# Kernel tuning notes

Hardware: AMD Instinct MI355X
Metric: run time of the kernel (lower is better)

Reference implementation:

```python
import jax, jax.numpy as jnp
import numpy as np

N_NODES = 100000
N_EDGES = 6400000


def setup_inputs() -> dict:
    key = jax.random.key(0)
    k = jax.random.split(key, 5)
    x = jax.random.normal(k[0], (N_NODES, 4), dtype=jnp.float32)
    edge_index = jax.random.randint(k[1], (2, N_EDGES), 0, N_NODES, dtype=jnp.int32)
    # Glorot-style init for GCN linear weights
    W1 = jax.random.normal(k[2], (4, 16), dtype=jnp.float32) * (1.0 / np.sqrt(4.0))
    b1 = jnp.zeros((16,), dtype=jnp.float32)
    W2 = jax.random.normal(k[3], (16, 2), dtype=jnp.float32) * (1.0 / np.sqrt(16.0))
    b2 = jnp.zeros((2,), dtype=jnp.float32)
    return {"x": x, "edge_index": edge_index, "W1": W1, "b1": b1, "W2": W2, "b2": b2}


def _gcn_conv(x, src, dst, deg_inv_sqrt, W, b):
    """One GCNConv layer: linear transform -> symmetric-normalized scatter-add -> bias.

    src, dst already include self-loops; deg_inv_sqrt precomputed on the
    self-loop-augmented graph (matches PyG GCNConv defaults).
    """
    n = x.shape[0]
    h = x @ W                                   # [N, F_out]
    coef = deg_inv_sqrt[src] * deg_inv_sqrt[dst]  # [E+N]
    msg = h[src] * coef[:, None]                # gather + scale, [E+N, F_out]
    out = jax.ops.segment_sum(msg, dst, num_segments=n)  # scatter-add
    return out + b


def reference(x, edge_index, W1, b1, W2, b2):
    n = x.shape[0]
    loop = jnp.arange(n, dtype=edge_index.dtype)
    src = jnp.concatenate([edge_index[0], loop])  # add self-loops
    dst = jnp.concatenate([edge_index[1], loop])
    deg = jax.ops.segment_sum(jnp.ones_like(dst, dtype=x.dtype), dst, num_segments=n)
    deg_inv_sqrt = jnp.where(deg > 0, jax.lax.rsqrt(deg), 0.0)

    h = jax.nn.relu(_gcn_conv(x, src, dst, deg_inv_sqrt, W1, b1))
    return _gcn_conv(h, src, dst, deg_inv_sqrt, W2, b2)
```

## Files before the change

### kernel.cpp

```cpp
#include <hip/hip_runtime.h>

#define TPB 256
#define CSH 10
#define CN 1024
#define NBC_MAX 128
#define STILE 8192
#define EPT (STILE / TPB)

#define B20 1048576
#define S1F 131072.0f
#define S2F 8192.0f

typedef unsigned long long u64;

__device__ __forceinline__ unsigned enc_fx(float v, float scale) {
    int xi = __float2int_rn(v * scale);
    xi = max(-(B20 - 1), min(B20 - 1, xi));
    return (unsigned)(xi + B20);
}

__global__ void k_zero(int* __restrict__ p, int n) {
    int i = blockIdx.x * blockDim.x + threadIdx.x;
    if (i < n) p[i] = 0;
}

__global__ void k_passCk(const int* __restrict__ src, const int* __restrict__ dst,
                         unsigned* __restrict__ packed, int* __restrict__ chunkl,
                         int* __restrict__ chunkp, int E, int NBC) {
    __shared__ unsigned stage[STILE];
    __shared__ int cnt[NBC_MAX], lb[NBC_MAX];
    int tb = blockIdx.x * STILE;
    int te = min(E, tb + STILE);
    if (threadIdx.x < NBC_MAX) cnt[threadIdx.x] = 0;
    __syncthreads();
    unsigned pk[EPT];
    int br[EPT];
#pragma unroll
    for (int u = 0; u < EPT; u++) {
        int i = tb + u * TPB + (int)threadIdx.x;
        br[u] = -1;
        if (i < te) {
            int d = dst[i];
            int b = d >> CSH;
            pk[u] = ((unsigned)src[i] << CSH) | (unsigned)(d & (CN - 1));
            int r = atomicAdd(&cnt[b], 1);
            br[u] = b | (r << 7);
        }
    }
    __syncthreads();
    if (threadIdx.x < (unsigned)NBC) {
        int b = threadIdx.x;
        int sum = 0;
        for (int j = 0; j < b; j++) sum += cnt[j];
        lb[b] = sum;
        chunkl[blockIdx.x * NBC + b] = cnt[b];
        chunkp[blockIdx.x * NBC + b] = tb + sum;
    }
    __syncthreads();
#pragma unroll
    for (int u = 0; u < EPT; u++) {
        if (br[u] >= 0) {
            int b = br[u] & (NBC_MAX - 1);
            stage[lb[b] + (br[u] >> 7)] = pk[u];
        }
    }
    __syncthreads();
    for (int i = threadIdx.x; i < te - tb; i += TPB)
        packed[tb + i] = stage[i];
}

__global__ void k_degk(const unsigned* __restrict__ packed, const int* __restrict__ chunkl,
                       const int* __restrict__ chunkp, int* __restrict__ deg,
                       int SD, int ntiles, int NBC, int N) {
    __shared__ int cnt[CN];
    for (int i = threadIdx.x; i < CN; i += TPB) cnt[i] = 0;
    __syncthreads();
    int b = blockIdx.x / SD, s = blockIdx.x - b * SD;
    int wv = threadIdx.x >> 6, lane = threadIdx.x & 63;
    for (int t = s * 4 + wv; t < ntiles; t += SD * 4) {
        int len = chunkl[t * NBC + b];
        if (!len) continue;
        int pos = chunkp[t * NBC + b];
        for (int i = lane; i < len; i += 64)
            atomicAdd(&cnt[packed[pos + i] & (CN - 1)], 1);
    }
    __syncthreads();
    int node0 = b << CSH;
    for (int i = threadIdx.x; i < CN; i += TPB)
        if (cnt[i] && node0 + i < N) atomicAdd(&deg[node0 + i], cnt[i]);
}

__global__ void k_prepv(const float* __restrict__ x, const int* __restrict__ deg,
                        float* __restrict__ xs, unsigned* __restrict__ xse, int N) {
    int v = blockIdx.x * blockDim.x + threadIdx.x;
    if (v >= N) return;
    float di = rsqrtf((float)(deg[v] + 1));
    float4 xv = ((const float4*)x)[v];
    xv.x *= di; xv.y *= di; xv.z *= di; xv.w *= di;
    ((float4*)xs)[v] = xv;
    uint4 e;
    e.x = enc_fx(xv.x, S1F); e.y = enc_fx(xv.y, S1F);
    e.z = enc_fx(xv.z, S1F); e.w = enc_fx(xv.w, S1F);
    ((uint4*)xse)[v] = e;
}

__global__ void k_agg1k(const unsigned* __restrict__ packed, const int* __restrict__ chunkl,
                        const int* __restrict__ chunkp, const unsigned* __restrict__ xse,
                        u64* __restrict__ partial1, int S1, int ntiles, int NBC) {
    __shared__ u64 acc[CN * 3];
    for (int i = threadIdx.x; i < CN * 3; i += TPB) acc[i] = 0ULL;
    __syncthreads();
    int b = blockIdx.x / S1, s = blockIdx.x - b * S1;
    int wv = threadIdx.x >> 6, lane = threadIdx.x & 63;
    for (int t = s * 4 + wv; t < ntiles; t += S1 * 4) {
        int len = chunkl[t * NBC + b];
        if (!len) continue;
        int pos = chunkp[t * NBC + b];
        for (int i = lane; i < len; i += 64) {
            unsigned pk = packed[pos + i];
            uint4 g = ((const uint4*)xse)[pk >> CSH];
            int n = pk & (CN - 1);
            atomicAdd(&acc[n * 3 + 0], (u64)g.x | ((u64)g.y << 32));
            atomicAdd(&acc[n * 3 + 1], (u64)g.z | ((u64)g.w << 32));
        }
    }
    __syncthreads();
    u64* p = partial1 + (size_t)blockIdx.x * (CN * 2);
    for (int i = threadIdx.x; i < CN * 2; i += TPB)
        p[i] = acc[(i >> 1) * 3 + (i & 1)];
}

__global__ void k_comb1q(const u64* __restrict__ partial1,
                         const float* __restrict__ xs, const int* __restrict__ deg,
                         const float* __restrict__ W1, const float* __restrict__ b1,
                         const float* __restrict__ W2,
                         float* __restrict__ hs2f, unsigned* __restrict__ hs2e,
                         int S1, int N) {
    __shared__ float w1[64], w2[32], bb[16];
    if (threadIdx.x < 64) w1[threadIdx.x] = W1[threadIdx.x];
    if (threadIdx.x < 32) w2[threadIdx.x] = W2[threadIdx.x];
    if (threadIdx.x < 16) bb[threadIdx.x] = b1[threadIdx.x];
    __syncthreads();
    int v = blockIdx.x * blockDim.x + threadIdx.x;
    if (v >= N) return;
    int b = v >> CSH, lv = v & (CN - 1);
    u64 a01 = 0, a23 = 0;
    for (int s = 0; s < S1; s++) {
        const u64* q = partial1 + ((size_t)(b * S1 + s) * CN + lv) * 2;
        a01 += q[0];
        a23 += q[1];
    }
    int dg = deg[v];
    long long bias = (long long)dg << 20;
    const float inv = 1.0f / S1F;
    float f0 = (float)((long long)(a01 & 0xffffffffULL) - bias) * inv;
    float f1 = (float)((long long)(a01 >> 32) - bias) * inv;
    float f2 = (float)((long long)(a23 & 0xffffffffULL) - bias) * inv;
    float f3 = (float)((long long)(a23 >> 32) - bias) * inv;
    float4 self = ((const float4*)xs)[v];
    float di = rsqrtf((float)(dg + 1));
    float v0 = (f0 + self.x) * di, v1 = (f1 + self.y) * di;
    float v2 = (f2 + self.z) * di, v3 = (f3 + self.w) * di;
    float s0 = 0.f, s1 = 0.f;
#pragma unroll
    for (int j = 0; j < 16; j++) {
        float h = v0 * w1[j] + v1 * w1[16 + j] + v2 * w1[32 + j] + v3 * w1[48 + j] + bb[j];
        h = fmaxf(h, 0.0f);
        s0 += h * w2[2 * j];
        s1 += h * w2[2 * j + 1];
    }
    s0 *= di; s1 *= di;
    ((float2*)hs2f)[v] = make_float2(s0, s1);
    uint2 e;
    e.x = enc_fx(s0, S2F);
    e.y = enc_fx(s1, S2F);
    ((uint2*)hs2e)[v] = e;
}

__global__ void k_agg2k(const unsigned* __restrict__ packed, const int* __restrict__ chunkl,
                        const int* __restrict__ chunkp, const unsigned* __restrict__ hs2e,
                        u64* __restrict__ partial2, int S2, int ntiles, int NBC) {
    __shared__ u64 acc[CN];
    for (int i = threadIdx.x; i < CN; i += TPB) acc[i] = 0ULL;
    __syncthreads();
    int b = blockIdx.x / S2, s = blockIdx.x - b * S2;
    int wv = threadIdx.x >> 6, lane = threadIdx.x & 63;
    for (int t = s * 4 + wv; t < ntiles; t += S2 * 4) {
        int len = chunkl[t * NBC + b];
        if (!len) continue;
        int pos = chunkp[t * NBC + b];
        for (int i = lane; i < len; i += 64) {
            unsigned pk = packed[pos + i];
            uint2 g = ((const uint2*)hs2e)[pk >> CSH];
            atomicAdd(&acc[pk & (CN - 1)], (u64)g.x | ((u64)g.y << 32));
        }
    }
    __syncthreads();
    u64* p = partial2 + (size_t)blockIdx.x * CN;
    for (int i = threadIdx.x; i < CN; i += TPB) p[i] = acc[i];
}

__global__ void k_comb2q(const u64* __restrict__ partial2,
                         const float* __restrict__ hs2f, const int* __restrict__ deg,
                         const float* __restrict__ b2, float* __restrict__ out,
                         int S2, int N) {
    int v = blockIdx.x * blockDim.x + threadIdx.x;
    if (v >= N) return;
    int b = v >> CSH, lv = v & (CN - 1);
    u64 t = 0;
    for (int s = 0; s < S2; s++)
        t += partial2[(size_t)(b * S2 + s) * CN + lv];
    int dg = deg[v];
    long long bias = (long long)dg << 20;
    const float inv = 1.0f / S2F;
    float f0 = (float)((long long)(t & 0xffffffffULL) - bias) * inv;
    float f1 = (float)((long long)(t >> 32) - bias) * inv;
    float2 self = ((const float2*)hs2f)[v];
    float di = rsqrtf((float)(dg + 1));
    ((float2*)out)[v] = make_float2((f0 + self.x) * di + b2[0],
                                    (f1 + self.y) * di + b2[1]);
}


__global__ void k_deg_fb(const int* __restrict__ dst, int* __restrict__ deg, int E) {
    int i = blockIdx.x * blockDim.x + threadIdx.x;
    if (i < E) atomicAdd(&deg[dst[i]], 1);
}
__global__ void k_dis_fb(const int* __restrict__ deg, float* __restrict__ dis, int N) {
    int v = blockIdx.x * blockDim.x + threadIdx.x;
    if (v < N) dis[v] = rsqrtf((float)(deg[v] + 1));
}
__global__ void k_lin1_fb(const float* __restrict__ x, const float* __restrict__ W1,
// ... 53 lines not shown
    int s = src[e], d = dst[e];
    float2 m = ((const float2*)hs2)[s];
    atomicAdd(&agg2[d * 2 + 0], m.x);
    atomicAdd(&agg2[d * 2 + 1], m.y);
}
__global__ void k_out_fb(const float* __restrict__ agg2, const float* __restrict__ dis,
                         const float* __restrict__ b2, float* __restrict__ out, int N) {
    int v = blockIdx.x * blockDim.x + threadIdx.x;
    if (v >= N) return;
    float d = dis[v];
    out[v * 2 + 0] = agg2[v * 2 + 0] * d + b2[0];
    out[v * 2 + 1] = agg2[v * 2 + 1] * d + b2[1];
}


extern "C" void kernel_launch(void* const* d_in, const int* in_sizes, int n_in,
                              void* d_out, int out_size, void* d_ws, size_t ws_size,
                              hipStream_t stream) {
    const float* x  = (const float*)d_in[0];
    const int*   ei = (const int*)d_in[1];
    const float* W1 = (const float*)d_in[2];
    const float* b1 = (const float*)d_in[3];
    const float* W2 = (const float*)d_in[4];
    const float* b2 = (const float*)d_in[5];

    const int N = in_sizes[0] / 4;
    const int E = in_sizes[1] / 2;
    const int* src = ei;
    const int* dst = ei + E;
    float* outp = (float*)d_out;

    auto align = [](size_t v) { return (v + 255) & ~(size_t)255; };
    const int NBC = (N + CN - 1) >> CSH;
    const int gN  = (N + TPB - 1) / TPB;
    const int ntiles = (E + STILE - 1) / STILE;
    const int SD = 8;
    const bool src_fits = (size_t)N <= ((size_t)1 << (32 - CSH));
    const bool fx_safe = (long long)E <= (long long)N * 512;

    const int S1 = 8, S2 = 16;
    size_t part_bytes  = (size_t)NBC * S1 * CN * 16;
    size_t part2_bytes = (size_t)NBC * S2 * CN * 8;
    size_t part_max = part_bytes > part2_bytes ? part_bytes : part2_bytes;

    size_t need_new = align((size_t)E * 4)
                    + align((size_t)N * 16)
                    + align((size_t)N * 16)
                    + align((size_t)N * 8)
                    + align((size_t)N * 8)
                    + align((size_t)N * 4)
                    + align((size_t)ntiles * NBC * 4)
                    + align((size_t)ntiles * NBC * 4)
                    + align(part_max);

    if (ws_size >= need_new && NBC <= NBC_MAX && src_fits && fx_safe) {
        char* ws = (char*)d_ws;
        unsigned* packed = (unsigned*)ws; ws += align((size_t)E * 4);
        float* xs    = (float*)ws;    ws += align((size_t)N * 16);
        unsigned* xse = (unsigned*)ws; ws += align((size_t)N * 16);
        float* hs2f  = (float*)ws;    ws += align((size_t)N * 8);
        unsigned* hs2e = (unsigned*)ws; ws += align((size_t)N * 8);
        int* deg     = (int*)ws;      ws += align((size_t)N * 4);
        int* chunkl  = (int*)ws;      ws += align((size_t)ntiles * NBC * 4);
        int* chunkp  = (int*)ws;      ws += align((size_t)ntiles * NBC * 4);
        u64* partial1 = (u64*)ws;
        u64* partial2 = (u64*)ws;

        k_zero<<<gN, TPB, 0, stream>>>(deg, N);
        k_passCk<<<ntiles, TPB, 0, stream>>>(src, dst, packed, chunkl, chunkp, E, NBC);
        k_degk<<<NBC * SD, TPB, 0, stream>>>(packed, chunkl, chunkp, deg, SD, ntiles, NBC, N);
        k_prepv<<<gN, TPB, 0, stream>>>(x, deg, xs, xse, N);
        k_agg1k<<<NBC * S1, TPB, 0, stream>>>(packed, chunkl, chunkp, xse, partial1, S1, ntiles, NBC);
        k_comb1q<<<gN, TPB, 0, stream>>>(partial1, xs, deg, W1, b1, W2, hs2f, hs2e, S1, N);
        k_agg2k<<<NBC * S2, TPB, 0, stream>>>(packed, chunkl, chunkp, hs2e, partial2, S2, ntiles, NBC);
        k_comb2q<<<gN, TPB, 0, stream>>>(partial2, hs2f, deg, b2, outp, S2, N);
    } else {
        char* ws = (char*)d_ws;
        int*   deg  = (int*)ws;   ws += align((size_t)N * 4);
        float* dis  = (float*)ws; ws += align((size_t)N * 4);
        float* hs1  = (float*)ws; ws += align((size_t)N * 16 * 4);
        float* agg1 = (float*)ws; ws += align((size_t)N * 16 * 4);
        float* hs2  = (float*)ws; ws += align((size_t)N * 2 * 4);
        float* agg2 = (float*)ws; ws += align((size_t)N * 2 * 4);
        int gE = (E + TPB - 1) / TPB;
        int gE4 = ((size_t)E * 4 + TPB - 1) / TPB;

        k_zero<<<gN, TPB, 0, stream>>>(deg, N);
        k_deg_fb<<<gE, TPB, 0, stream>>>(dst, deg, E);
        k_dis_fb<<<gN, TPB, 0, stream>>>(deg, dis, N);
        k_lin1_fb<<<gN, TPB, 0, stream>>>(x, W1, dis, hs1, agg1, N);
        k_scat1_fb<<<gE4, TPB, 0, stream>>>(src, dst, hs1, agg1, E * 4);
        k_lin2_fb<<<gN, TPB, 0, stream>>>(agg1, dis, b1, W2, hs2, agg2, N);
        k_scat2_fb<<<gE, TPB, 0, stream>>>(src, dst, hs2, agg2, E);
        k_out_fb<<<gN, TPB, 0, stream>>>(agg2, dis, b2, outp, N);
    }
}
```

Before: 241.1 us.

## Transpose chunk metadata, batch-load chunk descriptors, and unroll gathers for latency hiding

The chunk length and position tables are stored bucket-major so each wave reads a contiguous range of chunk descriptors. Waves load 64 descriptors at once, broadcast them with shuffles, and process two chunks per iteration with four independent packed and feature loads issued before the atomics. This is meant to hide gather latency by raising memory-level parallelism. It also doubles the split factors S1 and S2 when workspace allows, giving more blocks but larger partial buffers and more combine work.

```diff
diff --git a/kernel.cpp b/kernel.cpp
--- a/kernel.cpp
+++ b/kernel.cpp
@@ -25,8 +25,8 @@
 }
 
 __global__ void k_passCk(const int* __restrict__ src, const int* __restrict__ dst,
-                         unsigned* __restrict__ packed, int* __restrict__ chunkl,
-                         int* __restrict__ chunkp, int E, int NBC) {
+                         unsigned* __restrict__ packed, int* __restrict__ chunklT,
+                         int* __restrict__ chunkpT, int E, int NBC, int ntiles) {
     __shared__ unsigned stage[STILE];
     __shared__ int cnt[NBC_MAX], lb[NBC_MAX];
     int tb = blockIdx.x * STILE;
@@ -53,8 +53,8 @@
         int sum = 0;
         for (int j = 0; j < b; j++) sum += cnt[j];
         lb[b] = sum;
-        chunkl[blockIdx.x * NBC + b] = cnt[b];
-        chunkp[blockIdx.x * NBC + b] = tb + sum;
+        chunklT[(size_t)b * ntiles + blockIdx.x] = cnt[b];
+        chunkpT[(size_t)b * ntiles + blockIdx.x] = tb + sum;
     }
     __syncthreads();
 #pragma unroll
@@ -69,20 +69,45 @@
         packed[tb + i] = stage[i];
 }
 
-__global__ void k_degk(const unsigned* __restrict__ packed, const int* __restrict__ chunkl,
-                       const int* __restrict__ chunkp, int* __restrict__ deg,
-                       int SD, int ntiles, int NBC, int N) {
+
+__global__ void k_degk(const unsigned* __restrict__ packed, const int* __restrict__ chunklT,
+                       const int* __restrict__ chunkpT, int* __restrict__ deg,
+                       int SD, int ntiles, int E, int N) {
     __shared__ int cnt[CN];
     for (int i = threadIdx.x; i < CN; i += TPB) cnt[i] = 0;
     __syncthreads();
     int b = blockIdx.x / SD, s = blockIdx.x - b * SD;
     int wv = threadIdx.x >> 6, lane = threadIdx.x & 63;
-    for (int t = s * 4 + wv; t < ntiles; t += SD * 4) {
-        int len = chunkl[t * NBC + b];
-        if (!len) continue;
-        int pos = chunkp[t * NBC + b];
-        for (int i = lane; i < len; i += 64)
-            atomicAdd(&cnt[packed[pos + i] & (CN - 1)], 1);
+    int W = SD * 4, widx = s * 4 + wv;
+    int base = ntiles / W, rem = ntiles - base * W;
+    int q0 = widx * base + min(widx, rem);
+    int nch = base + (widx < rem ? 1 : 0);
+    const int* cl = chunklT + (size_t)b * ntiles;
+    const int* cp = chunkpT + (size_t)b * ntiles;
+    for (int jb = 0; jb < nch; jb += 64) {
+        int mylen = 0, mypos = 0;
+        if (jb + lane < nch) {
+            mylen = cl[q0 + jb + lane];
+            mypos = cp[q0 + jb + lane];
+        }
+        int jcnt = min(64, nch - jb);
+        for (int j = 0; j < jcnt; j += 2) {
+            int len0 = __shfl(mylen, j), pos0 = __shfl(mypos, j);
+            int len1 = 0, pos1 = 0;
+            if (j + 1 < jcnt) { len1 = __shfl(mylen, j + 1); pos1 = __shfl(mypos, j + 1); }
+            unsigned pk0a = packed[min(pos0 + lane,      E - 1)];
+            unsigned pk0b = packed[min(pos0 + 64 + lane, E - 1)];
+            unsigned pk1a = packed[min(pos1 + lane,      E - 1)];
+            unsigned pk1b = packed[min(pos1 + 64 + lane, E - 1)];
+            if (lane < len0)      atomicAdd(&cnt[pk0a & (CN - 1)], 1);
+            if (64 + lane < len0) atomicAdd(&cnt[pk0b & (CN - 1)], 1);
+            if (lane < len1)      atomicAdd(&cnt[pk1a & (CN - 1)], 1);
+            if (64 + lane < len1) atomicAdd(&cnt[pk1b & (CN - 1)], 1);
+            for (int i = 128 + lane; i < len0; i += 64)
+                atomicAdd(&cnt[packed[pos0 + i] & (CN - 1)], 1);
+            for (int i = 128 + lane; i < len1; i += 64)
+                atomicAdd(&cnt[packed[pos1 + i] & (CN - 1)], 1);
+        }
     }
     __syncthreads();
     int node0 = b << CSH;
@@ -104,24 +129,58 @@
     ((uint4*)xse)[v] = e;
 }
 
-__global__ void k_agg1k(const unsigned* __restrict__ packed, const int* __restrict__ chunkl,
-                        const int* __restrict__ chunkp, const unsigned* __restrict__ xse,
-                        u64* __restrict__ partial1, int S1, int ntiles, int NBC) {
+#define AGG1_AT(pkv, gv) { int n_ = (int)((pkv) & (CN - 1)) * 3; \
+    atomicAdd(&acc[n_],     (u64)(gv).x | ((u64)(gv).y << 32)); \
+    atomicAdd(&acc[n_ + 1], (u64)(gv).z | ((u64)(gv).w << 32)); }
+
+__global__ void k_agg1k(const unsigned* __restrict__ packed, const int* __restrict__ chunklT,
+                        const int* __restrict__ chunkpT, const unsigned* __restrict__ xse,
+                        u64* __restrict__ partial1, int S1, int ntiles, int E) {
     __shared__ u64 acc[CN * 3];
     for (int i = threadIdx.x; i < CN * 3; i += TPB) acc[i] = 0ULL;
     __syncthreads();
     int b = blockIdx.x / S1, s = blockIdx.x - b * S1;
     int wv = threadIdx.x >> 6, lane = threadIdx.x & 63;
-    for (int t = s * 4 + wv; t < ntiles; t += S1 * 4) {
-        int len = chunkl[t * NBC + b];
-        if (!len) continue;
-        int pos = chunkp[t * NBC + b];
-        for (int i = lane; i < len; i += 64) {
-            unsigned pk = packed[pos + i];
-            uint4 g = ((const uint4*)xse)[pk >> CSH];
-            int n = pk & (CN - 1);
-            atomicAdd(&acc[n * 3 + 0], (u64)g.x | ((u64)g.y << 32));
-            atomicAdd(&acc[n * 3 + 1], (u64)g.z | ((u64)g.w << 32));
+    int W = S1 * 4, widx = s * 4 + wv;
+    int base = ntiles / W, rem = ntiles - base * W;
+    int q0 = widx * base + min(widx, rem);
+    int nch = base + (widx < rem ? 1 : 0);
+    const int* cl = chunklT + (size_t)b * ntiles;
+    const int* cp = chunkpT + (size_t)b * ntiles;
+    const uint4* xse4 = (const uint4*)xse;
+    for (int jb = 0; jb < nch; jb += 64) {
+        int mylen = 0, mypos = 0;
+        if (jb + lane < nch) {
+            mylen = cl[q0 + jb + lane];
+            mypos = cp[q0 + jb + lane];
+        }
+        int jcnt = min(64, nch - jb);
+        for (int j = 0; j < jcnt; j += 2) {
+            int len0 = __shfl(mylen, j), pos0 = __shfl(mypos, j);
+            int len1 = 0, pos1 = 0;
+            if (j + 1 < jcnt) { len1 = __shfl(mylen, j + 1); pos1 = __shfl(mypos, j + 1); }
+            unsigned pk0a = packed[min(pos0 + lane,      E - 1)];
+            unsigned pk0b = packed[min(pos0 + 64 + lane, E - 1)];
+            unsigned pk1a = packed[min(pos1 + lane,      E - 1)];
+            unsigned pk1b = packed[min(pos1 + 64 + lane, E - 1)];
+            uint4 g0a = xse4[pk0a >> CSH];
+            uint4 g0b = xse4[pk0b >> CSH];
+            uint4 g1a = xse4[pk1a >> CSH];
+            uint4 g1b = xse4[pk1b >> CSH];
+            if (lane < len0)      AGG1_AT(pk0a, g0a);
+            if (64 + lane < len0) AGG1_AT(pk0b, g0b);
+            if (lane < len1)      AGG1_AT(pk1a, g1a);
+            if (64 + lane < len1) AGG1_AT(pk1b, g1b);
+            for (int i = 128 + lane; i < len0; i += 64) {
+                unsigned pk = packed[pos0 + i];
+                uint4 g = xse4[pk >> CSH];
+                AGG1_AT(pk, g);
+            }
+            for (int i = 128 + lane; i < len1; i += 64) {
+                unsigned pk = packed[pos1 + i];
+                uint4 g = xse4[pk >> CSH];
+                AGG1_AT(pk, g);
+            }
         }
     }
     __syncthreads();
@@ -177,22 +236,58 @@
     ((uint2*)hs2e)[v] = e;
 }
 
-__global__ void k_agg2k(const unsigned* __restrict__ packed, const int* __restrict__ chunkl,
-                        const int* __restrict__ chunkp, const unsigned* __restrict__ hs2e,
-                        u64* __restrict__ partial2, int S2, int ntiles, int NBC) {
+__global__ void k_agg2k(const unsigned* __restrict__ packed, const int* __restrict__ chunklT,
+                        const int* __restrict__ chunkpT, const unsigned* __restrict__ hs2e,
+                        u64* __restrict__ partial2, int S2, int ntiles, int E) {
     __shared__ u64 acc[CN];
     for (int i = threadIdx.x; i < CN; i += TPB) acc[i] = 0ULL;
     __syncthreads();
     int b = blockIdx.x / S2, s = blockIdx.x - b * S2;
     int wv = threadIdx.x >> 6, lane = threadIdx.x & 63;
-    for (int t = s * 4 + wv; t < ntiles; t += S2 * 4) {
-        int len = chunkl[t * NBC + b];
-        if (!len) continue;
-        int pos = chunkp[t * NBC + b];
-        for (int i = lane; i < len; i += 64) {
-            unsigned pk = packed[pos + i];
-            uint2 g = ((const uint2*)hs2e)[pk >> CSH];
-            atomicAdd(&acc[pk & (CN - 1)], (u64)g.x | ((u64)g.y << 32));
+    int W = S2 * 4, widx = s * 4 + wv;
+    int base = ntiles / W, rem = ntiles - base * W;
+    int q0 = widx * base + min(widx, rem);
+    int nch = base + (widx < rem ? 1 : 0);
+    const int* cl = chunklT + (size_t)b * ntiles;
+    const int* cp = chunkpT + (size_t)b * ntiles;
+    const uint2* h2 = (const uint2*)hs2e;
+    for (int jb = 0; jb < nch; jb += 64) {
+        int mylen = 0, mypos = 0;
+        if (jb + lane < nch) {
+            mylen = cl[q0 + jb + lane];
+            mypos = cp[q0 + jb + lane];
+        }
+        int jcnt = min(64, nch - jb);
+        for (int j = 0; j < jcnt; j += 2) {
+            int len0 = __shfl(mylen, j), pos0 = __shfl(mypos, j);
+            int len1 = 0, pos1 = 0;
+            if (j + 1 < jcnt) { len1 = __shfl(mylen, j + 1); pos1 = __shfl(mypos, j + 1); }
+            unsigned pk0a = packed[min(pos0 + lane,      E - 1)];
+            unsigned pk0b = packed[min(pos0 + 64 + lane, E - 1)];
+            unsigned pk1a = packed[min(pos1 + lane,      E - 1)];
+            unsigned pk1b = packed[min(pos1 + 64 + lane, E - 1)];
+            uint2 g0a = h2[pk0a >> CSH];
+            uint2 g0b = h2[pk0b >> CSH];
+            uint2 g1a = h2[pk1a >> CSH];
+            uint2 g1b = h2[pk1b >> CSH];
+            if (lane < len0)
+                atomicAdd(&acc[pk0a & (CN - 1)], (u64)g0a.x | ((u64)g0a.y << 32));
+            if (64 + lane < len0)
+                atomicAdd(&acc[pk0b & (CN - 1)], (u64)g0b.x | ((u64)g0b.y << 32));
+            if (lane < len1)
+                atomicAdd(&acc[pk1a & (CN - 1)], (u64)g1a.x | ((u64)g1a.y << 32));
+            if (64 + lane < len1)
+                atomicAdd(&acc[pk1b & (CN - 1)], (u64)g1b.x | ((u64)g1b.y << 32));
+            for (int i = 128 + lane; i < len0; i += 64) {
+                unsigned pk = packed[pos0 + i];
+                uint2 g = h2[pk >> CSH];
+                atomicAdd(&acc[pk & (CN - 1)], (u64)g.x | ((u64)g.y << 32));
+            }
+            for (int i = 128 + lane; i < len1; i += 64) {
+                unsigned pk = packed[pos1 + i];
+                uint2 g = h2[pk >> CSH];
+                atomicAdd(&acc[pk & (CN - 1)], (u64)g.x | ((u64)g.y << 32));
+            }
         }
     }
     __syncthreads();
@@ -323,20 +418,28 @@
     const bool src_fits = (size_t)N <= ((size_t)1 << (32 - CSH));
     const bool fx_safe = (long long)E <= (long long)N * 512;
 
-    const int S1 = 8, S2 = 16;
+    auto calc_need = [&](int S1v, int S2v) {
+        size_t p1 = (size_t)NBC * S1v * CN * 16;
+        size_t p2 = (size_t)NBC * S2v * CN * 8;
+        size_t pm = p1 > p2 ? p1 : p2;
+        return align((size_t)E * 4)
+             + align((size_t)N * 16)
+             + align((size_t)N * 16)
+             + align((size_t)N * 8)
+             + align((size_t)N * 8)
+             + align((size_t)N * 4)
+             + align((size_t)ntiles * NBC * 4)
+             + align((size_t)ntiles * NBC * 4)
+             + align(pm);
+    };
+
+    int S1 = 16, S2 = 32;
+    size_t need_new = calc_need(S1, S2);
+    if (ws_size < need_new) { S1 = 8; S2 = 16; need_new = calc_need(S1, S2); }
+
     size_t part_bytes  = (size_t)NBC * S1 * CN * 16;
     size_t part2_bytes = (size_t)NBC * S2 * CN * 8;
     size_t part_max = part_bytes > part2_bytes ? part_bytes : part2_bytes;
-
-    size_t need_new = align((size_t)E * 4)
-                    + align((size_t)N * 16)
-                    + align((size_t)N * 16)
-                    + align((size_t)N * 8)
-                    + align((size_t)N * 8)
-                    + align((size_t)N * 4)
-                    + align((size_t)ntiles * NBC * 4)
-                    + align((size_t)ntiles * NBC * 4)
-                    + align(part_max);
 
     if (ws_size >= need_new && NBC <= NBC_MAX && src_fits && fx_safe) {
         char* ws = (char*)d_ws;
@@ -346,18 +449,19 @@
         float* hs2f  = (float*)ws;    ws += align((size_t)N * 8);
         unsigned* hs2e = (unsigned*)ws; ws += align((size_t)N * 8);
         int* deg     = (int*)ws;      ws += align((size_t)N * 4);
-        int* chunkl  = (int*)ws;      ws += align((size_t)ntiles * NBC * 4);
-        int* chunkp  = (int*)ws;      ws += align((size_t)ntiles * NBC * 4);
+        int* chunklT = (int*)ws;      ws += align((size_t)ntiles * NBC * 4);
+        int* chunkpT = (int*)ws;      ws += align((size_t)ntiles * NBC * 4);
         u64* partial1 = (u64*)ws;
         u64* partial2 = (u64*)ws;
+        (void)part_max;
 
         k_zero<<<gN, TPB, 0, stream>>>(deg, N);
-        k_passCk<<<ntiles, TPB, 0, stream>>>(src, dst, packed, chunkl, chunkp, E, NBC);
-        k_degk<<<NBC * SD, TPB, 0, stream>>>(packed, chunkl, chunkp, deg, SD, ntiles, NBC, N);
+        k_passCk<<<ntiles, TPB, 0, stream>>>(src, dst, packed, chunklT, chunkpT, E, NBC, ntiles);
+        k_degk<<<NBC * SD, TPB, 0, stream>>>(packed, chunklT, chunkpT, deg, SD, ntiles, E, N);
         k_prepv<<<gN, TPB, 0, stream>>>(x, deg, xs, xse, N);
-        k_agg1k<<<NBC * S1, TPB, 0, stream>>>(packed, chunkl, chunkp, xse, partial1, S1, ntiles, NBC);
+        k_agg1k<<<NBC * S1, TPB, 0, stream>>>(packed, chunklT, chunkpT, xse, partial1, S1, ntiles, E);
         k_comb1q<<<gN, TPB, 0, stream>>>(partial1, xs, deg, W1, b1, W2, hs2f, hs2e, S1, N);
-        k_agg2k<<<NBC * S2, TPB, 0, stream>>>(packed, chunkl, chunkp, hs2e, partial2, S2, ntiles, NBC);
+        k_agg2k<<<NBC * S2, TPB, 0, stream>>>(packed, chunklT, chunkpT, hs2e, partial2, S2, ntiles, E);
         k_comb2q<<<gN, TPB, 0, stream>>>(partial2, hs2f, deg, b2, outp, S2, N);
     } else {
         char* ws = (char*)d_ws;
```

Result: slower. 254.4 us (+5.5%).

## Add second-level source-bucket sort to edges for locality in aggregation gathers

Applied to the files above, without the earlier changes.

Adds a second partitioning pass that sorts each destination bucket's edges by source super-bucket (256 nodes), using a histogram, scans and an LDS-buffered scatter into a new packed2 array. The aggregation kernels then stream contiguous per-bucket edge ranges with 4x unrolled gathers, so feature gathers hit nearby source nodes and are intended to get better cache locality. It also transposes the chunk metadata, raises S1 to 16 and reuses the packed buffer for the partials. The cost is several extra kernel launches and one more full read and write of the edge list.

```diff
diff --git a/kernel.cpp b/kernel.cpp
--- a/kernel.cpp
+++ b/kernel.cpp
@@ -7,6 +7,11 @@
 #define STILE 8192
 #define EPT (STILE / TPB)
 
+#define P2 8
+#define SB_SH 8
+#define SBN_MAX 512
+#define CAP 28
+
 #define B20 1048576
 #define S1F 131072.0f
 #define S2F 8192.0f
@@ -25,8 +30,8 @@
 }
 
 __global__ void k_passCk(const int* __restrict__ src, const int* __restrict__ dst,
-                         unsigned* __restrict__ packed, int* __restrict__ chunkl,
-                         int* __restrict__ chunkp, int E, int NBC) {
+                         unsigned* __restrict__ packed, int* __restrict__ chunklT,
+                         int* __restrict__ chunkpT, int E, int NBC, int ntiles) {
     __shared__ unsigned stage[STILE];
     __shared__ int cnt[NBC_MAX], lb[NBC_MAX];
     int tb = blockIdx.x * STILE;
@@ -53,8 +58,8 @@
         int sum = 0;
         for (int j = 0; j < b; j++) sum += cnt[j];
         lb[b] = sum;
-        chunkl[blockIdx.x * NBC + b] = cnt[b];
-        chunkp[blockIdx.x * NBC + b] = tb + sum;
+        chunklT[(size_t)b * ntiles + blockIdx.x] = cnt[b];
+        chunkpT[(size_t)b * ntiles + blockIdx.x] = tb + sum;
     }
     __syncthreads();
 #pragma unroll
@@ -69,25 +74,145 @@
         packed[tb + i] = stage[i];
 }
 
-__global__ void k_degk(const unsigned* __restrict__ packed, const int* __restrict__ chunkl,
-                       const int* __restrict__ chunkp, int* __restrict__ deg,
-                       int SD, int ntiles, int NBC, int N) {
-    __shared__ int cnt[CN];
-    for (int i = threadIdx.x; i < CN; i += TPB) cnt[i] = 0;
-    __syncthreads();
-    int b = blockIdx.x / SD, s = blockIdx.x - b * SD;
+__global__ void k_p2a(const unsigned* __restrict__ packed, const int* __restrict__ chunklT,
+                      const int* __restrict__ chunkpT, int* __restrict__ h,
+                      int* __restrict__ deg, int ntiles, int SBN, int N) {
+    __shared__ int hist[SBN_MAX];
+    __shared__ int dcnt[CN];
+    int b = blockIdx.x / P2, p = blockIdx.x - b * P2;
+    for (int i = threadIdx.x; i < SBN_MAX; i += TPB) hist[i] = 0;
+    for (int i = threadIdx.x; i < CN; i += TPB) dcnt[i] = 0;
+    __syncthreads();
+    int t0 = (int)((long long)ntiles * p / P2);
+    int t1 = (int)((long long)ntiles * (p + 1) / P2);
     int wv = threadIdx.x >> 6, lane = threadIdx.x & 63;
-    for (int t = s * 4 + wv; t < ntiles; t += SD * 4) {
-        int len = chunkl[t * NBC + b];
+    const int* cl = chunklT + (size_t)b * ntiles;
+    const int* cp = chunkpT + (size_t)b * ntiles;
+    for (int t = t0 + wv; t < t1; t += 4) {
+        int len = cl[t];
         if (!len) continue;
-        int pos = chunkp[t * NBC + b];
-        for (int i = lane; i < len; i += 64)
-            atomicAdd(&cnt[packed[pos + i] & (CN - 1)], 1);
-    }
-    __syncthreads();
+        int pos = cp[t];
+        for (int i = lane; i < len; i += 64) {
+            unsigned pk = packed[pos + i];
+            atomicAdd(&hist[pk >> (CSH + SB_SH)], 1);
+            atomicAdd(&dcnt[pk & (CN - 1)], 1);
+        }
+    }
+    __syncthreads();
+    int* hp = h + (size_t)blockIdx.x * SBN;
+    for (int i = threadIdx.x; i < SBN; i += TPB) hp[i] = hist[i];
     int node0 = b << CSH;
     for (int i = threadIdx.x; i < CN; i += TPB)
-        if (cnt[i] && node0 + i < N) atomicAdd(&deg[node0 + i], cnt[i]);
+        if (dcnt[i] && node0 + i < N) atomicAdd(&deg[node0 + i], dcnt[i]);
+}
+
+__global__ void k_scan1(const int* __restrict__ h, int* __restrict__ bsize, int SBN) {
+    __shared__ int red[TPB];
+    int b = blockIdx.x;
+    const int* hb = h + (size_t)b * P2 * SBN;
+    int n = P2 * SBN;
+    int sum = 0;
+    for (int i = threadIdx.x; i < n; i += TPB) sum += hb[i];
+    red[threadIdx.x] = sum;
+    __syncthreads();
+    for (int off = TPB / 2; off > 0; off >>= 1) {
+        if (threadIdx.x < off) red[threadIdx.x] += red[threadIdx.x + off];
+        __syncthreads();
+    }
+    if (threadIdx.x == 0) bsize[b] = red[0];
+}
+
+__global__ void k_scanbase(const int* __restrict__ bsize, int* __restrict__ base, int NBC) {
+    __shared__ int s[NBC_MAX];
+    int t = threadIdx.x;
+    if (t < NBC_MAX) s[t] = (t < NBC) ? bsize[t] : 0;
+    __syncthreads();
+    for (int off = 1; off < NBC_MAX; off <<= 1) {
+        int v = 0;
+        if (t < NBC_MAX && t >= off) v = s[t - off];
+        __syncthreads();
+        if (t < NBC_MAX) s[t] += v;
+        __syncthreads();
+    }
+    if (t < NBC) base[t] = (t == 0) ? 0 : s[t - 1];
+    if (t == 0) base[NBC] = s[NBC - 1];
+}
+
+__global__ void k_scan3(int* __restrict__ h, const int* __restrict__ base, int SBN) {
+    __shared__ int tsum[TPB];
+    int b = blockIdx.x;
+    int* hb = h + (size_t)b * P2 * SBN;
+    int n = SBN * P2;
+    int per = (n + TPB - 1) / TPB;
+    int i0 = threadIdx.x * per;
+    int vals[16];
+    int sum = 0;
+    for (int k = 0; k < per; k++) {
+        int idx = i0 + k;
+        int v = 0;
+        if (idx < n) {
+            int sb = idx >> 3, p = idx & (P2 - 1);
+            v = hb[p * SBN + sb];
+        }
+        vals[k] = v;
+        sum += v;
+    }
+    tsum[threadIdx.x] = sum;
+    __syncthreads();
+    for (int off = 1; off < TPB; off <<= 1) {
+        int v = (threadIdx.x >= off) ? tsum[threadIdx.x - off] : 0;
+        __syncthreads();
+        tsum[threadIdx.x] += v;
+        __syncthreads();
+    }
+    int run = base[b] + ((threadIdx.x == 0) ? 0 : tsum[threadIdx.x - 1]);
+    for (int k = 0; k < per; k++) {
+        int idx = i0 + k;
+        if (idx < n) {
+            int sb = idx >> 3, p = idx & (P2 - 1);
+            hb[p * SBN + sb] = run;
+            run += vals[k];
+        }
+    }
+}
+
+__global__ void k_p2b(const unsigned* __restrict__ packed, const int* __restrict__ chunklT,
+                      const int* __restrict__ chunkpT, const int* __restrict__ off,
+                      unsigned* __restrict__ packed2, int ntiles, int SBN) {
+    __shared__ unsigned binbuf[SBN_MAX * CAP];
+    __shared__ int cnt[SBN_MAX];
+    __shared__ int goff[SBN_MAX];
+    int b = blockIdx.x / P2, p = blockIdx.x - b * P2;
+    const int* offp = off + (size_t)blockIdx.x * SBN;
+    for (int i = threadIdx.x; i < SBN_MAX; i += TPB) {
+        cnt[i] = 0;
+        goff[i] = (i < SBN) ? offp[i] : 0;
+    }
+    __syncthreads();
+    int t0 = (int)((long long)ntiles * p / P2);
+    int t1 = (int)((long long)ntiles * (p + 1) / P2);
+    int wv = threadIdx.x >> 6, lane = threadIdx.x & 63;
+    const int* cl = chunklT + (size_t)b * ntiles;
+    const int* cp = chunkpT + (size_t)b * ntiles;
+    for (int t = t0 + wv; t < t1; t += 4) {
+        int len = cl[t];
+        if (!len) continue;
+        int pos = cp[t];
+        for (int i = lane; i < len; i += 64) {
+            unsigned pk = packed[pos + i];
+            int sb = pk >> (CSH + SB_SH);
+            int r = atomicAdd(&cnt[sb], 1);
+            if (r < CAP) binbuf[sb * CAP + r] = pk;
+            else packed2[goff[sb] + r] = pk;
+        }
+    }
+    __syncthreads();
+    for (int sb = wv; sb < SBN; sb += 4) {
+        int c = min(cnt[sb], CAP);
+        int gb = goff[sb];
+        for (int i = lane; i < c; i += 64)
+            packed2[gb + i] = binbuf[sb * CAP + i];
+    }
 }
 
 __global__ void k_prepv(const float* __restrict__ x, const int* __restrict__ deg,
@@ -104,30 +229,41 @@
     ((uint4*)xse)[v] = e;
 }
 
-__global__ void k_agg1k(const unsigned* __restrict__ packed, const int* __restrict__ chunkl,
-                        const int* __restrict__ chunkp, const unsigned* __restrict__ xse,
-                        u64* __restrict__ partial1, int S1, int ntiles, int NBC) {
+#define AGG1_AT(pkv, gv) { int n_ = (int)((pkv) & (CN - 1)) * 3; \
+    atomicAdd(&acc[n_],     (u64)(gv).x | ((u64)(gv).y << 32)); \
+    atomicAdd(&acc[n_ + 1], (u64)(gv).z | ((u64)(gv).w << 32)); }
+
+__global__ void k_agg1n(const unsigned* __restrict__ packed2, const int* __restrict__ base,
+                        const unsigned* __restrict__ xse, u64* __restrict__ partial1, int S1) {
     __shared__ u64 acc[CN * 3];
     for (int i = threadIdx.x; i < CN * 3; i += TPB) acc[i] = 0ULL;
     __syncthreads();
     int b = blockIdx.x / S1, s = blockIdx.x - b * S1;
-    int wv = threadIdx.x >> 6, lane = threadIdx.x & 63;
-    for (int t = s * 4 + wv; t < ntiles; t += S1 * 4) {
-        int len = chunkl[t * NBC + b];
-        if (!len) continue;
-        int pos = chunkp[t * NBC + b];
-        for (int i = lane; i < len; i += 64) {
-            unsigned pk = packed[pos + i];
-            uint4 g = ((const uint4*)xse)[pk >> CSH];
-            int n = pk & (CN - 1);
-            atomicAdd(&acc[n * 3 + 0], (u64)g.x | ((u64)g.y << 32));
-            atomicAdd(&acc[n * 3 + 1], (u64)g.z | ((u64)g.w << 32));
-        }
+    int lo = base[b], sz = base[b + 1] - lo;
+    int i0 = lo + (int)((long long)sz * s / S1);
+    int i1 = lo + (int)((long long)sz * (s + 1) / S1);
+    const uint4* xse4 = (const uint4*)xse;
+    int i = i0 + (int)threadIdx.x;
+    for (; i + 3 * TPB < i1; i += 4 * TPB) {
+        unsigned pa = packed2[i];
+        unsigned pb = packed2[i + TPB];
+        unsigned pc = packed2[i + 2 * TPB];
+        unsigned pd = packed2[i + 3 * TPB];
+        uint4 ga = xse4[pa >> CSH];
+        uint4 gb = xse4[pb >> CSH];
+        uint4 gc = xse4[pc >> CSH];
+        uint4 gd = xse4[pd >> CSH];
+        AGG1_AT(pa, ga); AGG1_AT(pb, gb); AGG1_AT(pc, gc); AGG1_AT(pd, gd);
+    }
+    for (; i < i1; i += TPB) {
+        unsigned pk = packed2[i];
+        uint4 g = xse4[pk >> CSH];
+        AGG1_AT(pk, g);
     }
     __syncthreads();
     u64* p = partial1 + (size_t)blockIdx.x * (CN * 2);
-    for (int i = threadIdx.x; i < CN * 2; i += TPB)
-        p[i] = acc[(i >> 1) * 3 + (i & 1)];
+    for (int i2 = threadIdx.x; i2 < CN * 2; i2 += TPB)
+        p[i2] = acc[(i2 >> 1) * 3 + (i2 & 1)];
 }
 
 __global__ void k_comb1q(const u64* __restrict__ partial1,
@@ -177,27 +313,39 @@
     ((uint2*)hs2e)[v] = e;
 }
 
-__global__ void k_agg2k(const unsigned* __restrict__ packed, const int* __restrict__ chunkl,
-                        const int* __restrict__ chunkp, const unsigned* __restrict__ hs2e,
-                        u64* __restrict__ partial2, int S2, int ntiles, int NBC) {
+__global__ void k_agg2n(const unsigned* __restrict__ packed2, const int* __restrict__ base,
+                        const unsigned* __restrict__ hs2e, u64* __restrict__ partial2, int S2) {
     __shared__ u64 acc[CN];
     for (int i = threadIdx.x; i < CN; i += TPB) acc[i] = 0ULL;
     __syncthreads();
     int b = blockIdx.x / S2, s = blockIdx.x - b * S2;
-    int wv = threadIdx.x >> 6, lane = threadIdx.x & 63;
-    for (int t = s * 4 + wv; t < ntiles; t += S2 * 4) {
-        int len = chunkl[t * NBC + b];
-        if (!len) continue;
-        int pos = chunkp[t * NBC + b];
-        for (int i = lane; i < len; i += 64) {
-            unsigned pk = packed[pos + i];
-            uint2 g = ((const uint2*)hs2e)[pk >> CSH];
-            atomicAdd(&acc[pk & (CN - 1)], (u64)g.x | ((u64)g.y << 32));
-        }
+    int lo = base[b], sz = base[b + 1] - lo;
+    int i0 = lo + (int)((long long)sz * s / S2);
+    int i1 = lo + (int)((long long)sz * (s + 1) / S2);
+    const uint2* h2 = (const uint2*)hs2e;
+    int i = i0 + (int)threadIdx.x;
+    for (; i + 3 * TPB < i1; i += 4 * TPB) {
+        unsigned pa = packed2[i];
+        unsigned pb = packed2[i + TPB];
+        unsigned pc = packed2[i + 2 * TPB];
+        unsigned pd = packed2[i + 3 * TPB];
+        uint2 ga = h2[pa >> CSH];
+        uint2 gb = h2[pb >> CSH];
+        uint2 gc = h2[pc >> CSH];
+        uint2 gd = h2[pd >> CSH];
+        atomicAdd(&acc[pa & (CN - 1)], (u64)ga.x | ((u64)ga.y << 32));
+        atomicAdd(&acc[pb & (CN - 1)], (u64)gb.x | ((u64)gb.y << 32));
+        atomicAdd(&acc[pc & (CN - 1)], (u64)gc.x | ((u64)gc.y << 32));
+        atomicAdd(&acc[pd & (CN - 1)], (u64)gd.x | ((u64)gd.y << 32));
+    }
+    for (; i < i1; i += TPB) {
+        unsigned pk = packed2[i];
+        uint2 g = h2[pk >> CSH];
+        atomicAdd(&acc[pk & (CN - 1)], (u64)g.x | ((u64)g.y << 32));
     }
     __syncthreads();
     u64* p = partial2 + (size_t)blockIdx.x * CN;
-    for (int i = threadIdx.x; i < CN; i += TPB) p[i] = acc[i];
+    for (int i2 = threadIdx.x; i2 < CN; i2 += TPB) p[i2] = acc[i2];
 }
 
 __global__ void k_comb2q(const u64* __restrict__ partial2,
@@ -317,18 +465,21 @@
 
     auto align = [](size_t v) { return (v + 255) & ~(size_t)255; };
     const int NBC = (N + CN - 1) >> CSH;
+    const int SBN = (N + 255) >> SB_SH;
     const int gN  = (N + TPB - 1) / TPB;
     const int ntiles = (E + STILE - 1) / STILE;
-    const int SD = 8;
     const bool src_fits = (size_t)N <= ((size_t)1 << (32 - CSH));
     const bool fx_safe = (long long)E <= (long long)N * 512;
 
-    const int S1 = 8, S2 = 16;
-    size_t part_bytes  = (size_t)NBC * S1 * CN * 16;
+    const int S1 = 16, S2 = 16;
+    size_t part1_bytes = (size_t)NBC * S1 * CN * 16;
     size_t part2_bytes = (size_t)NBC * S2 * CN * 8;
-    size_t part_max = part_bytes > part2_bytes ? part_bytes : part2_bytes;
-
-    size_t need_new = align((size_t)E * 4)
+    size_t pkA_bytes = (size_t)E * 4;
+    if (part1_bytes > pkA_bytes) pkA_bytes = part1_bytes;
+    if (part2_bytes > pkA_bytes) pkA_bytes = part2_bytes;
+
+    size_t need_new = align(pkA_bytes)
+                    + align((size_t)E * 4)
                     + align((size_t)N * 16)
                     + align((size_t)N * 16)
                     + align((size_t)N * 8)
@@ -336,28 +487,39 @@
                     + align((size_t)N * 4)
                     + align((size_t)ntiles * NBC * 4)
                     + align((size_t)ntiles * NBC * 4)
-                    + align(part_max);
-
-    if (ws_size >= need_new && NBC <= NBC_MAX && src_fits && fx_safe) {
+                    + align((size_t)NBC * P2 * SBN * 4)
+                    + align((size_t)NBC * 4)
+                    + align((size_t)(NBC + 1) * 4);
+
+    if (ws_size >= need_new && NBC <= NBC_MAX && SBN <= SBN_MAX && src_fits && fx_safe) {
         char* ws = (char*)d_ws;
-        unsigned* packed = (unsigned*)ws; ws += align((size_t)E * 4);
+        unsigned* packed = (unsigned*)ws;
+        u64* partial1 = (u64*)ws;
+        u64* partial2 = (u64*)ws;
+        ws += align(pkA_bytes);
+        unsigned* packed2 = (unsigned*)ws; ws += align((size_t)E * 4);
         float* xs    = (float*)ws;    ws += align((size_t)N * 16);
         unsigned* xse = (unsigned*)ws; ws += align((size_t)N * 16);
         float* hs2f  = (float*)ws;    ws += align((size_t)N * 8);
         unsigned* hs2e = (unsigned*)ws; ws += align((size_t)N * 8);
         int* deg     = (int*)ws;      ws += align((size_t)N * 4);
-        int* chunkl  = (int*)ws;      ws += align((size_t)ntiles * NBC * 4);
-        int* chunkp  = (int*)ws;      ws += align((size_t)ntiles * NBC * 4);
-        u64* partial1 = (u64*)ws;
-        u64* partial2 = (u64*)ws;
+        int* chunklT = (int*)ws;      ws += align((size_t)ntiles * NBC * 4);
+        int* chunkpT = (int*)ws;      ws += align((size_t)ntiles * NBC * 4);
+        int* h       = (int*)ws;      ws += align((size_t)NBC * P2 * SBN * 4);
+        int* bsize   = (int*)ws;      ws += align((size_t)NBC * 4);
+        int* base    = (int*)ws;      ws += align((size_t)(NBC + 1) * 4);
 
         k_zero<<<gN, TPB, 0, stream>>>(deg, N);
-        k_passCk<<<ntiles, TPB, 0, stream>>>(src, dst, packed, chunkl, chunkp, E, NBC);
-        k_degk<<<NBC * SD, TPB, 0, stream>>>(packed, chunkl, chunkp, deg, SD, ntiles, NBC, N);
+        k_passCk<<<ntiles, TPB, 0, stream>>>(src, dst, packed, chunklT, chunkpT, E, NBC, ntiles);
+        k_p2a<<<NBC * P2, TPB, 0, stream>>>(packed, chunklT, chunkpT, h, deg, ntiles, SBN, N);
+        k_scan1<<<NBC, TPB, 0, stream>>>(h, bsize, SBN);
+        k_scanbase<<<1, TPB, 0, stream>>>(bsize, base, NBC);
+        k_scan3<<<NBC, TPB, 0, stream>>>(h, base, SBN);
+        k_p2b<<<NBC * P2, TPB, 0, stream>>>(packed, chunklT, chunkpT, h, packed2, ntiles, SBN);
         k_prepv<<<gN, TPB, 0, stream>>>(x, deg, xs, xse, N);
-        k_agg1k<<<NBC * S1, TPB, 0, stream>>>(packed, chunkl, chunkp, xse, partial1, S1, ntiles, NBC);
+        k_agg1n<<<NBC * S1, TPB, 0, stream>>>(packed2, base, xse, partial1, S1);
         k_comb1q<<<gN, TPB, 0, stream>>>(partial1, xs, deg, W1, b1, W2, hs2f, hs2e, S1, N);
-        k_agg2k<<<NBC * S2, TPB, 0, stream>>>(packed, chunkl, chunkp, hs2e, partial2, S2, ntiles, NBC);
+        k_agg2n<<<NBC * S2, TPB, 0, stream>>>(packed2, base, hs2e, partial2, S2);
         k_comb2q<<<gN, TPB, 0, stream>>>(partial2, hs2f, deg, b2, outp, S2, N);
     } else {
         char* ws = (char*)d_ws;
```

Result: slower. 273.6 us (+13.4%).

## Bucket edges contiguously via degree histogram scan and unrolled aggregation

Applied to the files above, without the earlier changes.

Degrees are now computed directly from dst with global atomics before any bucketing. Per-bucket sizes are then summed and scanned so the scatter kernel can reserve contiguous global ranges per destination bucket with atomics. This drops the per-tile chunk length and position tables and the packed-edge degree pass. The aggregation kernels can then stream contiguous slices with 8-way unrolled gathers to hide latency, and S1 is raised to 16. The cost is more kernel launches, global atomic contention on degree counts, and scattered writes when copying the packed edges out.

```diff
diff --git a/kernel.cpp b/kernel.cpp
--- a/kernel.cpp
+++ b/kernel.cpp
@@ -4,7 +4,7 @@
 #define CSH 10
 #define CN 1024
 #define NBC_MAX 128
-#define STILE 8192
+#define STILE 4096
 #define EPT (STILE / TPB)
 
 #define B20 1048576
@@ -24,11 +24,65 @@
     if (i < n) p[i] = 0;
 }
 
-__global__ void k_passCk(const int* __restrict__ src, const int* __restrict__ dst,
-                         unsigned* __restrict__ packed, int* __restrict__ chunkl,
-                         int* __restrict__ chunkp, int E, int NBC) {
+__global__ void k_degg_v(const int* __restrict__ dst, int* __restrict__ deg, int E4) {
+    int i = blockIdx.x * blockDim.x + threadIdx.x;
+    if (i >= E4) return;
+    int4 d4 = ((const int4*)dst)[i];
+    atomicAdd(&deg[d4.x], 1);
+    atomicAdd(&deg[d4.y], 1);
+    atomicAdd(&deg[d4.z], 1);
+    atomicAdd(&deg[d4.w], 1);
+}
+__global__ void k_degg_s(const int* __restrict__ dst, int* __restrict__ deg, int E) {
+    int stride = gridDim.x * blockDim.x;
+    for (int i = blockIdx.x * blockDim.x + threadIdx.x; i < E; i += stride)
+        atomicAdd(&deg[dst[i]], 1);
+}
+
+__global__ void k_bsum(const int* __restrict__ deg, int* __restrict__ bsize, int N) {
+    __shared__ int red[TPB];
+    int b = blockIdx.x;
+    int v0 = b << CSH;
+    int sum = 0;
+    for (int i = threadIdx.x; i < CN; i += TPB) {
+        int v = v0 + i;
+        if (v < N) sum += deg[v];
+    }
+    red[threadIdx.x] = sum;
+    __syncthreads();
+    for (int off = TPB / 2; off > 0; off >>= 1) {
+        if (threadIdx.x < off) red[threadIdx.x] += red[threadIdx.x + off];
+        __syncthreads();
+    }
+    if (threadIdx.x == 0) bsize[b] = red[0];
+}
+
+__global__ void k_scanbase(const int* __restrict__ bsize, int* __restrict__ base,
+                           int* __restrict__ cur, int NBC) {
+    __shared__ int s[NBC_MAX];
+    int t = threadIdx.x;
+    if (t < NBC_MAX) s[t] = (t < NBC) ? bsize[t] : 0;
+    __syncthreads();
+    for (int off = 1; off < NBC_MAX; off <<= 1) {
+        int v = 0;
+        if (t < NBC_MAX && t >= off) v = s[t - off];
+        __syncthreads();
+        if (t < NBC_MAX) s[t] += v;
+        __syncthreads();
+    }
+    if (t < NBC) {
+        int b = (t == 0) ? 0 : s[t - 1];
+        base[t] = b;
+        cur[t] = b;
+    }
+    if (t == 0) base[NBC] = s[NBC - 1];
+}
+
+__global__ void k_bscat(const int* __restrict__ src, const int* __restrict__ dst,
+                        int* __restrict__ cur, unsigned* __restrict__ packed,
+                        int E, int NBC) {
     __shared__ unsigned stage[STILE];
-    __shared__ int cnt[NBC_MAX], lb[NBC_MAX];
+    __shared__ int cnt[NBC_MAX], lb[NBC_MAX], resv[NBC_MAX];
     int tb = blockIdx.x * STILE;
     int te = min(E, tb + STILE);
     if (threadIdx.x < NBC_MAX) cnt[threadIdx.x] = 0;
@@ -53,8 +107,7 @@
         int sum = 0;
         for (int j = 0; j < b; j++) sum += cnt[j];
         lb[b] = sum;
-        chunkl[blockIdx.x * NBC + b] = cnt[b];
-        chunkp[blockIdx.x * NBC + b] = tb + sum;
+        resv[b] = cnt[b] ? atomicAdd(&cur[b], cnt[b]) : 0;
     }
     __syncthreads();
 #pragma unroll
@@ -65,29 +118,14 @@
         }
     }
     __syncthreads();
-    for (int i = threadIdx.x; i < te - tb; i += TPB)
-        packed[tb + i] = stage[i];
-}
-
-__global__ void k_degk(const unsigned* __restrict__ packed, const int* __restrict__ chunkl,
-                       const int* __restrict__ chunkp, int* __restrict__ deg,
-                       int SD, int ntiles, int NBC, int N) {
-    __shared__ int cnt[CN];
-    for (int i = threadIdx.x; i < CN; i += TPB) cnt[i] = 0;
-    __syncthreads();
-    int b = blockIdx.x / SD, s = blockIdx.x - b * SD;
     int wv = threadIdx.x >> 6, lane = threadIdx.x & 63;
-    for (int t = s * 4 + wv; t < ntiles; t += SD * 4) {
-        int len = chunkl[t * NBC + b];
-        if (!len) continue;
-        int pos = chunkp[t * NBC + b];
-        for (int i = lane; i < len; i += 64)
-            atomicAdd(&cnt[packed[pos + i] & (CN - 1)], 1);
-    }
-    __syncthreads();
-    int node0 = b << CSH;
-    for (int i = threadIdx.x; i < CN; i += TPB)
-        if (cnt[i] && node0 + i < N) atomicAdd(&deg[node0 + i], cnt[i]);
+    for (int b = wv; b < NBC; b += 4) {
+        int c = cnt[b];
+        if (!c) continue;
+        int gb = resv[b], s0 = lb[b];
+        for (int i = lane; i < c; i += 64)
+            packed[gb + i] = stage[s0 + i];
+    }
 }
 
 __global__ void k_prepv(const float* __restrict__ x, const int* __restrict__ deg,
@@ -104,30 +142,39 @@
     ((uint4*)xse)[v] = e;
 }
 
-__global__ void k_agg1k(const unsigned* __restrict__ packed, const int* __restrict__ chunkl,
-                        const int* __restrict__ chunkp, const unsigned* __restrict__ xse,
-                        u64* __restrict__ partial1, int S1, int ntiles, int NBC) {
+#define AGG1_AT(pkv, gv) { int n_ = (int)((pkv) & (CN - 1)) * 3; \
+    atomicAdd(&acc[n_],     (u64)(gv).x | ((u64)(gv).y << 32)); \
+    atomicAdd(&acc[n_ + 1], (u64)(gv).z | ((u64)(gv).w << 32)); }
+
+__global__ void k_agg1u(const unsigned* __restrict__ packed, const int* __restrict__ base,
+                        const unsigned* __restrict__ xse, u64* __restrict__ partial1, int S1) {
     __shared__ u64 acc[CN * 3];
     for (int i = threadIdx.x; i < CN * 3; i += TPB) acc[i] = 0ULL;
     __syncthreads();
     int b = blockIdx.x / S1, s = blockIdx.x - b * S1;
-    int wv = threadIdx.x >> 6, lane = threadIdx.x & 63;
-    for (int t = s * 4 + wv; t < ntiles; t += S1 * 4) {
-        int len = chunkl[t * NBC + b];
-        if (!len) continue;
-        int pos = chunkp[t * NBC + b];
-        for (int i = lane; i < len; i += 64) {
-            unsigned pk = packed[pos + i];
-            uint4 g = ((const uint4*)xse)[pk >> CSH];
-            int n = pk & (CN - 1);
-            atomicAdd(&acc[n * 3 + 0], (u64)g.x | ((u64)g.y << 32));
-            atomicAdd(&acc[n * 3 + 1], (u64)g.z | ((u64)g.w << 32));
-        }
-    }
-    __syncthreads();
-    u64* p = partial1 + (size_t)blockIdx.x * (CN * 2);
-    for (int i = threadIdx.x; i < CN * 2; i += TPB)
-        p[i] = acc[(i >> 1) * 3 + (i & 1)];
+    int lo = base[b], sz = base[b + 1] - lo;
+    int i0 = lo + (int)((long long)sz * s / S1);
+    int i1 = lo + (int)((long long)sz * (s + 1) / S1);
+    const uint4* xse4 = (const uint4*)xse;
+    int iend = i1 - 1;
+    for (int i = i0 + (int)threadIdx.x; i < i1; i += 8 * TPB) {
+        unsigned p[8];
+        uint4 g[8];
+#pragma unroll
+        for (int k = 0; k < 8; k++) {
+            int idx = i + k * TPB;
+            p[k] = packed[min(idx, iend)];
+            g[k] = xse4[p[k] >> CSH];
+        }
+#pragma unroll
+        for (int k = 0; k < 8; k++) {
+            if (i + k * TPB < i1) AGG1_AT(p[k], g[k]);
+        }
+    }
+    __syncthreads();
+    u64* pp = partial1 + (size_t)blockIdx.x * (CN * 2);
+    for (int i2 = threadIdx.x; i2 < CN * 2; i2 += TPB)
+        pp[i2] = acc[(i2 >> 1) * 3 + (i2 & 1)];
 }
 
 __global__ void k_comb1q(const u64* __restrict__ partial1,
@@ -177,27 +224,35 @@
     ((uint2*)hs2e)[v] = e;
 }
 
-__global__ void k_agg2k(const unsigned* __restrict__ packed, const int* __restrict__ chunkl,
-                        const int* __restrict__ chunkp, const unsigned* __restrict__ hs2e,
-                        u64* __restrict__ partial2, int S2, int ntiles, int NBC) {
+__global__ void k_agg2u(const unsigned* __restrict__ packed, const int* __restrict__ base,
+                        const unsigned* __restrict__ hs2e, u64* __restrict__ partial2, int S2) {
     __shared__ u64 acc[CN];
     for (int i = threadIdx.x; i < CN; i += TPB) acc[i] = 0ULL;
     __syncthreads();
     int b = blockIdx.x / S2, s = blockIdx.x - b * S2;
-    int wv = threadIdx.x >> 6, lane = threadIdx.x & 63;
-    for (int t = s * 4 + wv; t < ntiles; t += S2 * 4) {
-        int len = chunkl[t * NBC + b];
-        if (!len) continue;
-        int pos = chunkp[t * NBC + b];
-        for (int i = lane; i < len; i += 64) {
-            unsigned pk = packed[pos + i];
-            uint2 g = ((const uint2*)hs2e)[pk >> CSH];
-            atomicAdd(&acc[pk & (CN - 1)], (u64)g.x | ((u64)g.y << 32));
-        }
-    }
-    __syncthreads();
-    u64* p = partial2 + (size_t)blockIdx.x * CN;
-    for (int i = threadIdx.x; i < CN; i += TPB) p[i] = acc[i];
+    int lo = base[b], sz = base[b + 1] - lo;
+    int i0 = lo + (int)((long long)sz * s / S2);
+    int i1 = lo + (int)((long long)sz * (s + 1) / S2);
+    const uint2* h2 = (const uint2*)hs2e;
+    int iend = i1 - 1;
+    for (int i = i0 + (int)threadIdx.x; i < i1; i += 8 * TPB) {
+        unsigned p[8];
+        uint2 g[8];
+#pragma unroll
+        for (int k = 0; k < 8; k++) {
+            int idx = i + k * TPB;
+            p[k] = packed[min(idx, iend)];
+            g[k] = h2[p[k] >> CSH];
+        }
+#pragma unroll
+        for (int k = 0; k < 8; k++) {
+            if (i + k * TPB < i1)
+                atomicAdd(&acc[p[k] & (CN - 1)], (u64)g[k].x | ((u64)g[k].y << 32));
+        }
+    }
+    __syncthreads();
+    u64* pp = partial2 + (size_t)blockIdx.x * CN;
+    for (int i2 = threadIdx.x; i2 < CN; i2 += TPB) pp[i2] = acc[i2];
 }
 
 __global__ void k_comb2q(const u64* __restrict__ partial2,
@@ -319,45 +374,54 @@
     const int NBC = (N + CN - 1) >> CSH;
     const int gN  = (N + TPB - 1) / TPB;
     const int ntiles = (E + STILE - 1) / STILE;
-    const int SD = 8;
     const bool src_fits = (size_t)N <= ((size_t)1 << (32 - CSH));
     const bool fx_safe = (long long)E <= (long long)N * 512;
 
-    const int S1 = 8, S2 = 16;
-    size_t part_bytes  = (size_t)NBC * S1 * CN * 16;
+    const int S1 = 16, S2 = 16;
+    size_t part1_bytes = (size_t)NBC * S1 * CN * 16;
     size_t part2_bytes = (size_t)NBC * S2 * CN * 8;
-    size_t part_max = part_bytes > part2_bytes ? part_bytes : part2_bytes;
+    size_t part_max = part1_bytes > part2_bytes ? part1_bytes : part2_bytes;
 
     size_t need_new = align((size_t)E * 4)
+                    + align(part_max)
                     + align((size_t)N * 16)
                     + align((size_t)N * 16)
                     + align((size_t)N * 8)
                     + align((size_t)N * 8)
                     + align((size_t)N * 4)
-                    + align((size_t)ntiles * NBC * 4)
-                    + align((size_t)ntiles * NBC * 4)
-                    + align(part_max);
+                    + align((size_t)NBC * 4)
+                    + align((size_t)NBC * 4)
+                    + align((size_t)(NBC + 1) * 4);
 
     if (ws_size >= need_new && NBC <= NBC_MAX && src_fits && fx_safe) {
         char* ws = (char*)d_ws;
         unsigned* packed = (unsigned*)ws; ws += align((size_t)E * 4);
+        u64* partial1 = (u64*)ws;
+        u64* partial2 = (u64*)ws;
+        ws += align(part_max);
         float* xs    = (float*)ws;    ws += align((size_t)N * 16);
         unsigned* xse = (unsigned*)ws; ws += align((size_t)N * 16);
         float* hs2f  = (float*)ws;    ws += align((size_t)N * 8);
         unsigned* hs2e = (unsigned*)ws; ws += align((size_t)N * 8);
         int* deg     = (int*)ws;      ws += align((size_t)N * 4);
-        int* chunkl  = (int*)ws;      ws += align((size_t)ntiles * NBC * 4);
-        int* chunkp  = (int*)ws;      ws += align((size_t)ntiles * NBC * 4);
-        u64* partial1 = (u64*)ws;
-        u64* partial2 = (u64*)ws;
+        int* bsize   = (int*)ws;      ws += align((size_t)NBC * 4);
+        int* cur     = (int*)ws;      ws += align((size_t)NBC * 4);
+        int* base    = (int*)ws;      ws += align((size_t)(NBC + 1) * 4);
 
         k_zero<<<gN, TPB, 0, stream>>>(deg, N);
-        k_passCk<<<ntiles, TPB, 0, stream>>>(src, dst, packed, chunkl, chunkp, E, NBC);
-        k_degk<<<NBC * SD, TPB, 0, stream>>>(packed, chunkl, chunkp, deg, SD, ntiles, NBC, N);
+        if ((E & 3) == 0) {
+            int E4 = E >> 2;
+            k_degg_v<<<(E4 + TPB - 1) / TPB, TPB, 0, stream>>>(dst, deg, E4);
+        } else {
+            k_degg_s<<<2048, TPB, 0, stream>>>(dst, deg, E);
+        }
+        k_bsum<<<NBC, TPB, 0, stream>>>(deg, bsize, N);
+        k_scanbase<<<1, TPB, 0, stream>>>(bsize, base, cur, NBC);
         k_prepv<<<gN, TPB, 0, stream>>>(x, deg, xs, xse, N);
-        k_agg1k<<<NBC * S1, TPB, 0, stream>>>(packed, chunkl, chunkp, xse, partial1, S1, ntiles, NBC);
+        k_bscat<<<ntiles, TPB, 0, stream>>>(src, dst, cur, packed, E, NBC);
+        k_agg1u<<<NBC * S1, TPB, 0, stream>>>(packed, base, xse, partial1, S1);
         k_comb1q<<<gN, TPB, 0, stream>>>(partial1, xs, deg, W1, b1, W2, hs2f, hs2e, S1, N);
-        k_agg2k<<<NBC * S2, TPB, 0, stream>>>(packed, chunkl, chunkp, hs2e, partial2, S2, ntiles, NBC);
+        k_agg2u<<<NBC * S2, TPB, 0, stream>>>(packed, base, hs2e, partial2, S2);
         k_comb2q<<<gN, TPB, 0, stream>>>(partial2, hs2f, deg, b2, outp, S2, N);
     } else {
         char* ws = (char*)d_ws;
```

New measurement: 478.2 us. 98.3% more time.
